# Kernel tuning notes

Hardware: AMD Instinct MI355X
Metric: run time of the kernel (lower is better)

## Reference

```python
import jax, jax.numpy as jnp
import numpy as np

IGNORE_INDEX = -100


def setup_inputs() -> dict:
    key = jax.random.key(0)
    k1, k2, k3 = jax.random.split(key, 3)
    B, S, D, V = 4, 2048, 2048, 32000
    hidden_states = jax.random.normal(k1, (B, S, D), dtype=jnp.float32)
    lm_head_weight = jax.random.normal(k2, (V, D), dtype=jnp.float32) * (D ** -0.5)
    labels = jax.random.randint(k3, (B, S), 0, V, dtype=jnp.int64)
    return {"hidden_states": hidden_states, "lm_head_weight": lm_head_weight, "labels": labels}


def reference(hidden_states, lm_head_weight, labels):
    D = hidden_states.shape[-1]
    # causal LM shift: predict token t+1 from hidden state t
    h = hidden_states[..., :-1, :].astype(jnp.float32).reshape(-1, D)   # [N, D]
    t = labels[..., 1:].reshape(-1)                                     # [N]
    w = lm_head_weight.astype(jnp.float32)                              # [V, D]

    logits = jnp.einsum("nd,vd->nv", h, w)                              # [N, V]
    lse = jax.nn.logsumexp(logits, axis=-1)                             # [N]

    valid = t != IGNORE_INDEX
    safe_t = jnp.where(valid, t, 0)
    gold = jnp.take_along_axis(logits, safe_t[:, None], axis=-1)[:, 0]  # [N]

    nll = jnp.where(valid, lse - gold, 0.0)
    n_valid = jnp.maximum(jnp.sum(valid.astype(jnp.float32)), 1.0)
    return jnp.sum(nll) / n_valid
```

## Files before the change

### kernel.cpp

```cpp
#include <hip/hip_runtime.h>
#include <hip/hip_bf16.h>
#include <stdint.h>

#define IGNORE_INDEX (-100)

typedef __attribute__((ext_vector_type(8))) short bf16x8;
typedef __attribute__((ext_vector_type(4))) float f32x4;

static constexpr int Bv = 4, Sv = 2048, Dv = 2048, Vv = 32000;
static constexpr int Nv = Bv * (Sv - 1);
static constexpr int NP = 8192;
static constexpr int TILE = 128;
static constexpr int BK = 64;

typedef const __attribute__((address_space(1))) unsigned int* gptr_t;
typedef __attribute__((address_space(3))) unsigned int* lptr_t;

__device__ __forceinline__ unsigned short f2bf(float f) {
    unsigned int u = __float_as_uint(f);
    u += 0x7fffu + ((u >> 16) & 1u);
    return (unsigned short)(u >> 16);
}

__global__ void convert_w_kernel(const float* __restrict__ w,
                                 unsigned short* __restrict__ wbf) {
    int i = blockIdx.x * blockDim.x + threadIdx.x;
    const float4 v = ((const float4*)w)[i];
    ushort4 o;
    o.x = f2bf(v.x); o.y = f2bf(v.y); o.z = f2bf(v.z); o.w = f2bf(v.w);
    ((ushort4*)wbf)[i] = o;
}

__global__ void convert_h_kernel(const float* __restrict__ h,
                                 unsigned short* __restrict__ hbf) {
    int i = blockIdx.x * blockDim.x + threadIdx.x;
    int e0 = i * 4;
    int n = e0 >> 11;
    int d = e0 & 2047;
    ushort4 o;
    if (n < Nv) {
        int b = n / 2047;
        int s = n - b * 2047;
        const float4 v = *(const float4*)(h + ((size_t)b * Sv + s) * Dv + d);
        o.x = f2bf(v.x); o.y = f2bf(v.y); o.z = f2bf(v.z); o.w = f2bf(v.w);
    } else {
        o.x = 0; o.y = 0; o.z = 0; o.w = 0;
    }
    ((ushort4*)hbf)[i] = o;
}

__global__ void prep_meta_kernel(const int* __restrict__ labels,
                                 int* __restrict__ t,
                                 float* __restrict__ sumexp,
                                 float* __restrict__ gold) {
    int n = blockIdx.x * blockDim.x + threadIdx.x;
    if (n >= NP) return;
    sumexp[n] = 0.0f;
    gold[n] = 0.0f;
    int tv = IGNORE_INDEX;
    if (n < Nv) {
        int b = n / 2047;
        int s = n - b * 2047;
        tv = labels[b * Sv + s + 1];
    }
    t[n] = tv;
}

__global__ __launch_bounds__(256, 2)
void ce_gemm(const unsigned short* __restrict__ hbf,
             const unsigned short* __restrict__ wbf,
             const int* __restrict__ t,
             float* __restrict__ sumexp,
             float* __restrict__ gold) {
    __shared__ unsigned short lds_a[TILE * BK];
    __shared__ unsigned short lds_b[TILE * BK];
    __shared__ float lds_rowsum[TILE];
    __shared__ int lds_t[TILE];

    const int tid  = threadIdx.x;
    const int lane = tid & 63;
    const int wave = tid >> 6;
    const int r    = wave >> 1;
    const int c    = wave & 1;
    const int quad = lane >> 4;
    const int l15  = lane & 15;
    const int R0   = blockIdx.x * TILE;
    const int C0   = blockIdx.y * TILE;

    f32x4 acc[4][4];
    const f32x4 z = {0.f, 0.f, 0.f, 0.f};
#pragma unroll
    for (int mi = 0; mi < 4; ++mi)
#pragma unroll
        for (int ni = 0; ni < 4; ++ni)
            acc[mi][ni] = z;

    const int ld_r = tid >> 3;
    const int jg   = (tid & 7) ^ (ld_r & 7);
    const int ld_c = jg * 8;
    const unsigned short* ga = hbf + (size_t)(R0 + ld_r) * Dv + ld_c;
    const unsigned short* gb = wbf + (size_t)(C0 + ld_r) * Dv + ld_c;
    unsigned short* la = lds_a + tid * 8;
    unsigned short* lb = lds_b + tid * 8;

    for (int k0 = 0; k0 < Dv; k0 += BK) {
        __syncthreads();
#pragma unroll
        for (int i = 0; i < 4; ++i) {
            __builtin_amdgcn_global_load_lds(
                (gptr_t)(ga + (size_t)i * 32 * Dv + k0),
                (lptr_t)(la + i * 2048), 16, 0, 0);
            __builtin_amdgcn_global_load_lds(
                (gptr_t)(gb + (size_t)i * 32 * Dv + k0),
                (lptr_t)(lb + i * 2048), 16, 0, 0);
        }
        __syncthreads();
#pragma unroll
        for (int ks = 0; ks < BK; ks += 32) {
            bf16x8 af[4], bfr[4];
            const int cbase = quad + (ks >> 3);
#pragma unroll
            for (int mi = 0; mi < 4; ++mi) {
                const int arow = r * 64 + mi * 16 + l15;
                af[mi] = *(const bf16x8*)(lds_a + arow * BK + ((cbase ^ (arow & 7)) * 8));
            }
#pragma unroll
            for (int ni = 0; ni < 4; ++ni) {
                const int brow = c * 64 + ni * 16 + l15;
                bfr[ni] = *(const bf16x8*)(lds_b + brow * BK + ((cbase ^ (brow & 7)) * 8));
            }
#pragma unroll
            for (int mi = 0; mi < 4; ++mi)
#pragma unroll
                for (int ni = 0; ni < 4; ++ni)
                    acc[mi][ni] = __builtin_amdgcn_mfma_f32_16x16x32_bf16(
                        af[mi], bfr[ni], acc[mi][ni], 0, 0, 0);
        }
    }

    __syncthreads();
    if (tid < TILE) {
        lds_rowsum[tid] = 0.0f;
        lds_t[tid] = t[R0 + tid];
    }
    __syncthreads();

#pragma unroll
    for (int mi = 0; mi < 4; ++mi) {
#pragma unroll
        for (int reg = 0; reg < 4; ++reg) {
            const int lrow = r * 64 + mi * 16 + quad * 4 + reg;
            const int grow = R0 + lrow;
            const int lbl  = lds_t[lrow];
            float s = 0.0f;
#pragma unroll
            for (int ni = 0; ni < 4; ++ni) {
                const float v = acc[mi][ni][reg];
                s += __expf(v);
                const int gcol = C0 + c * 64 + ni * 16 + l15;
                if (lbl == gcol) gold[grow] = v;
            }
#pragma unroll
            for (int off = 1; off < 16; off <<= 1)
                s += __shfl_xor(s, off, 64);
            if (l15 == 0) atomicAdd(&lds_rowsum[lrow], s);
        }
    }
    __syncthreads();
    if (tid < TILE) {
        const int grow = R0 + tid;
        if (grow < Nv) atomicAdd(&sumexp[grow], lds_rowsum[tid]);
    }
}

__global__ void ce_finalize(const float* __restrict__ sumexp,
                            const float* __restrict__ gold,
                            const int* __restrict__ t,
                            float* __restrict__ out) {
    __shared__ float ssum[4];
    __shared__ float scnt[4];
    float s = 0.0f, cnt = 0.0f;
    for (int n = threadIdx.x; n < Nv; n += 256) {
        if (t[n] != IGNORE_INDEX) {
            s += logf(sumexp[n]) - gold[n];
            cnt += 1.0f;
        }
    }
#pragma unroll
    for (int off = 32; off > 0; off >>= 1) {
        s += __shfl_down(s, off, 64);
        cnt += __shfl_down(cnt, off, 64);
    }
    const int wid = threadIdx.x >> 6;
    if ((threadIdx.x & 63) == 0) { ssum[wid] = s; scnt[wid] = cnt; }
    __syncthreads();
    if (threadIdx.x == 0) {
        float S = 0.0f, C = 0.0f;
        for (int i = 0; i < 4; ++i) { S += ssum[i]; C += scnt[i]; }
        out[0] = S / fmaxf(C, 1.0f);
    }
}

extern "C" void kernel_launch(void* const* d_in, const int* in_sizes, int n_in,
                              void* d_out, int out_size, void* d_ws, size_t ws_size,
                              hipStream_t stream) {
    const float* h      = (const float*)d_in[0];
    const float* w      = (const float*)d_in[1];
    const int*   labels = (const int*)d_in[2];
    float* out = (float*)d_out;

    char* ws = (char*)d_ws;
    unsigned short* hbf = (unsigned short*)ws;
    unsigned short* wbf = (unsigned short*)(ws + (size_t)NP * Dv * 2);
    char* tail = ws + (size_t)NP * Dv * 2 + (size_t)Vv * Dv * 2;
    float* sumexp = (float*)tail;
    float* gold   = (float*)(tail + (size_t)NP * 4);
    int*   t      = (int*)(tail + (size_t)NP * 8);

    hipLaunchKernelGGL(convert_w_kernel, dim3((Vv * Dv / 4) / 256), dim3(256), 0, stream, w, wbf);
    hipLaunchKernelGGL(convert_h_kernel, dim3((NP * Dv / 4) / 256), dim3(256), 0, stream, h, hbf);
    hipLaunchKernelGGL(prep_meta_kernel, dim3(NP / 256), dim3(256), 0, stream, labels, t, sumexp, gold);
    hipLaunchKernelGGL(ce_gemm, dim3(NP / TILE, Vv / TILE), dim3(256), 0, stream,
                       hbf, wbf, t, sumexp, gold);
    hipLaunchKernelGGL(ce_finalize, dim3(1), dim3(256), 0, stream, sumexp, gold, t, out);
}
```

Baseline: 1.347 ms.

## Enlarge GEMM tile to 256x256 with double-buffered async LDS prefetch

Grows the fused CE GEMM block tile from 128x128 to 256x256 with 512 threads, each wave computing 128x64. Adds a two-stage LDS double buffer that keeps the next K tile's global_load_lds in flight while MFMAs run on the current tile, with explicit vmcnt waits and barriers. Also raises wave priority around the MFMA section. The aim is more operand reuse per global byte and hiding load latency. In exchange it uses more LDS (128KB) and registers per block, which may reduce occupancy. 8192/256 x 32000/256 gives exactly 125 column blocks, so there is no tail issue.

```diff
diff --git a/kernel.cpp b/kernel.cpp
--- a/kernel.cpp
+++ b/kernel.cpp
@@ -1,5 +1,4 @@
 #include <hip/hip_runtime.h>
-#include <hip/hip_bf16.h>
 #include <stdint.h>
 
 #define IGNORE_INDEX (-100)
@@ -10,8 +9,9 @@
 static constexpr int Bv = 4, Sv = 2048, Dv = 2048, Vv = 32000;
 static constexpr int Nv = Bv * (Sv - 1);
 static constexpr int NP = 8192;
-static constexpr int TILE = 128;
+static constexpr int BM = 256;
 static constexpr int BK = 64;
+static constexpr int NT = Dv / BK;
 
 typedef const __attribute__((address_space(1))) unsigned int* gptr_t;
 typedef __attribute__((address_space(3))) unsigned int* lptr_t;
@@ -66,90 +66,119 @@
     t[n] = tv;
 }
 
-__global__ __launch_bounds__(256, 2)
+__global__ __launch_bounds__(512, 2)
 void ce_gemm(const unsigned short* __restrict__ hbf,
              const unsigned short* __restrict__ wbf,
              const int* __restrict__ t,
              float* __restrict__ sumexp,
              float* __restrict__ gold) {
-    __shared__ unsigned short lds_a[TILE * BK];
-    __shared__ unsigned short lds_b[TILE * BK];
-    __shared__ float lds_rowsum[TILE];
-    __shared__ int lds_t[TILE];
+    __shared__ unsigned short lds_a[2][BM * BK];
+    __shared__ unsigned short lds_b[2][BM * BK];
+    __shared__ float lds_rowsum[BM];
+    __shared__ int lds_t[BM];
 
     const int tid  = threadIdx.x;
     const int lane = tid & 63;
     const int wave = tid >> 6;
-    const int r    = wave >> 1;
-    const int c    = wave & 1;
+    const int wr   = wave >> 2;
+    const int wc   = wave & 3;
     const int quad = lane >> 4;
     const int l15  = lane & 15;
-    const int R0   = blockIdx.x * TILE;
-    const int C0   = blockIdx.y * TILE;
-
-    f32x4 acc[4][4];
+    const int R0   = blockIdx.x * BM;
+    const int C0   = blockIdx.y * BM;
+
+    f32x4 acc[8][4];
     const f32x4 z = {0.f, 0.f, 0.f, 0.f};
 #pragma unroll
-    for (int mi = 0; mi < 4; ++mi)
+    for (int mi = 0; mi < 8; ++mi)
 #pragma unroll
         for (int ni = 0; ni < 4; ++ni)
             acc[mi][ni] = z;
 
     const int ld_r = tid >> 3;
     const int jg   = (tid & 7) ^ (ld_r & 7);
-    const int ld_c = jg * 8;
-    const unsigned short* ga = hbf + (size_t)(R0 + ld_r) * Dv + ld_c;
-    const unsigned short* gb = wbf + (size_t)(C0 + ld_r) * Dv + ld_c;
-    unsigned short* la = lds_a + tid * 8;
-    unsigned short* lb = lds_b + tid * 8;
-
-    for (int k0 = 0; k0 < Dv; k0 += BK) {
-        __syncthreads();
-#pragma unroll
-        for (int i = 0; i < 4; ++i) {
-            __builtin_amdgcn_global_load_lds(
-                (gptr_t)(ga + (size_t)i * 32 * Dv + k0),
-                (lptr_t)(la + i * 2048), 16, 0, 0);
-            __builtin_amdgcn_global_load_lds(
-                (gptr_t)(gb + (size_t)i * 32 * Dv + k0),
-                (lptr_t)(lb + i * 2048), 16, 0, 0);
-        }
-        __syncthreads();
-#pragma unroll
-        for (int ks = 0; ks < BK; ks += 32) {
-            bf16x8 af[4], bfr[4];
-            const int cbase = quad + (ks >> 3);
-#pragma unroll
-            for (int mi = 0; mi < 4; ++mi) {
-                const int arow = r * 64 + mi * 16 + l15;
-                af[mi] = *(const bf16x8*)(lds_a + arow * BK + ((cbase ^ (arow & 7)) * 8));
-            }
-#pragma unroll
-            for (int ni = 0; ni < 4; ++ni) {
-                const int brow = c * 64 + ni * 16 + l15;
-                bfr[ni] = *(const bf16x8*)(lds_b + brow * BK + ((cbase ^ (brow & 7)) * 8));
-            }
-#pragma unroll
-            for (int mi = 0; mi < 4; ++mi)
-#pragma unroll
-                for (int ni = 0; ni < 4; ++ni)
-                    acc[mi][ni] = __builtin_amdgcn_mfma_f32_16x16x32_bf16(
-                        af[mi], bfr[ni], acc[mi][ni], 0, 0, 0);
-        }
-    }
-
-    __syncthreads();
-    if (tid < TILE) {
+    const unsigned short* ga = hbf + (size_t)(R0 + ld_r) * Dv + jg * 8;
+    const unsigned short* gb = wbf + (size_t)(C0 + ld_r) * Dv + jg * 8;
+
+#define STAGE(kt, buf)                                                         \
+    do {                                                                       \
+        const int _k0 = (kt) * BK;                                             \
+        unsigned short* _la = &lds_a[(buf)][tid * 8];                          \
+        unsigned short* _lb = &lds_b[(buf)][tid * 8];                          \
+        _Pragma("unroll")                                                      \
+        for (int _i = 0; _i < 4; ++_i) {                                       \
+            __builtin_amdgcn_global_load_lds(                                  \
+                (gptr_t)(ga + (size_t)_i * 64 * Dv + _k0),                     \
+                (lptr_t)(_la + _i * 4096), 16, 0, 0);                          \
+            __builtin_amdgcn_global_load_lds(                                  \
+                (gptr_t)(gb + (size_t)_i * 64 * Dv + _k0),                     \
+                (lptr_t)(_lb + _i * 4096), 16, 0, 0);                          \
+        }                                                                      \
+    } while (0)
+
+    STAGE(0, 0);
+    STAGE(1, 1);
+    asm volatile("s_waitcnt vmcnt(8)" ::: "memory");
+    __builtin_amdgcn_s_barrier();
+
+    int cur = 0;
+    for (int kt = 0; kt < NT; ++kt) {
+        const unsigned short* ba = &lds_a[cur][0];
+        const unsigned short* bb = &lds_b[cur][0];
+
+        bf16x8 bfr[4][2];
+#pragma unroll
+        for (int ni = 0; ni < 4; ++ni) {
+            const int brow = wc * 64 + ni * 16 + l15;
+            const int sw = brow & 7;
+            bfr[ni][0] = *(const bf16x8*)(bb + brow * BK + ((quad ^ sw) * 8));
+            bfr[ni][1] = *(const bf16x8*)(bb + brow * BK + (((quad + 4) ^ sw) * 8));
+        }
+
+        __builtin_amdgcn_s_setprio(1);
+#pragma unroll
+        for (int mi = 0; mi < 8; ++mi) {
+            const int arow = wr * 128 + mi * 16 + l15;
+            const int sw = arow & 7;
+            bf16x8 a0 = *(const bf16x8*)(ba + arow * BK + ((quad ^ sw) * 8));
+            bf16x8 a1 = *(const bf16x8*)(ba + arow * BK + (((quad + 4) ^ sw) * 8));
+#pragma unroll
+            for (int ni = 0; ni < 4; ++ni)
+                acc[mi][ni] = __builtin_amdgcn_mfma_f32_16x16x32_bf16(
+                    a0, bfr[ni][0], acc[mi][ni], 0, 0, 0);
+#pragma unroll
+            for (int ni = 0; ni < 4; ++ni)
+                acc[mi][ni] = __builtin_amdgcn_mfma_f32_16x16x32_bf16(
+                    a1, bfr[ni][1], acc[mi][ni], 0, 0, 0);
+        }
+        __builtin_amdgcn_s_setprio(0);
+
+        asm volatile("s_waitcnt lgkmcnt(0)" ::: "memory");
+        __builtin_amdgcn_s_barrier();
+
+        if (kt + 2 < NT) {
+            STAGE(kt + 2, cur);
+            asm volatile("s_waitcnt vmcnt(8)" ::: "memory");
+        } else if (kt + 1 < NT) {
+            asm volatile("s_waitcnt vmcnt(0)" ::: "memory");
+        }
+        __builtin_amdgcn_s_barrier();
+        cur ^= 1;
+    }
+#undef STAGE
+
+    __syncthreads();
+    if (tid < BM) {
         lds_rowsum[tid] = 0.0f;
         lds_t[tid] = t[R0 + tid];
     }
     __syncthreads();
 
 #pragma unroll
-    for (int mi = 0; mi < 4; ++mi) {
+    for (int mi = 0; mi < 8; ++mi) {
 #pragma unroll
         for (int reg = 0; reg < 4; ++reg) {
-            const int lrow = r * 64 + mi * 16 + quad * 4 + reg;
+            const int lrow = wr * 128 + mi * 16 + quad * 4 + reg;
             const int grow = R0 + lrow;
             const int lbl  = lds_t[lrow];
             float s = 0.0f;
@@ -157,7 +186,7 @@
             for (int ni = 0; ni < 4; ++ni) {
                 const float v = acc[mi][ni][reg];
                 s += __expf(v);
-                const int gcol = C0 + c * 64 + ni * 16 + l15;
+                const int gcol = C0 + wc * 64 + ni * 16 + l15;
                 if (lbl == gcol) gold[grow] = v;
             }
 #pragma unroll
@@ -167,7 +196,7 @@
         }
     }
     __syncthreads();
-    if (tid < TILE) {
+    if (tid < BM) {
         const int grow = R0 + tid;
         if (grow < Nv) atomicAdd(&sumexp[grow], lds_rowsum[tid]);
     }
@@ -220,7 +249,7 @@
     hipLaunchKernelGGL(convert_w_kernel, dim3((Vv * Dv / 4) / 256), dim3(256), 0, stream, w, wbf);
     hipLaunchKernelGGL(convert_h_kernel, dim3((NP * Dv / 4) / 256), dim3(256), 0, stream, h, hbf);
     hipLaunchKernelGGL(prep_meta_kernel, dim3(NP / 256), dim3(256), 0, stream, labels, t, sumexp, gold);
-    hipLaunchKernelGGL(ce_gemm, dim3(NP / TILE, Vv / TILE), dim3(256), 0, stream,
+    hipLaunchKernelGGL(ce_gemm, dim3(NP / BM, Vv / BM), dim3(512), 0, stream,
                        hbf, wbf, t, sumexp, gold);
     hipLaunchKernelGGL(ce_finalize, dim3(1), dim3(256), 0, stream, sumexp, gold, t, out);
 }
```

Result: slower. 1.597 ms (+18.6%).
